# Kernel tuning notes

Measured on AMD Instinct MI355X. Metric: run time of the kernel, lower is better.

## Reference

```python
import jax, jax.numpy as jnp
import numpy as np

BATCH = 4096
DIM = 256
TEMP = 0.5
COS_EPS = 1e-8  # torch.nn.CosineSimilarity default eps


def setup_inputs() -> dict:
    key = jax.random.key(0)
    k1, k2 = jax.random.split(key)
    zis = jax.random.normal(k1, (BATCH, DIM), dtype=jnp.float32)
    zjs = jax.random.normal(k2, (BATCH, DIM), dtype=jnp.float32)
    return {"zis": zis, "zjs": zjs}


def reference(zis, zjs):
    n = zis.shape[0]  # batch_size
    # representations = cat([zjs, zis]) -> (2N, D)
    reps = jnp.concatenate([zjs, zis], axis=0)
    # cosine similarity matrix: dot / max(|x||y|, eps)  (matches torch CosineSimilarity)
    norms = jnp.linalg.norm(reps, axis=-1)  # (2N,)
    sim = (reps @ reps.T) / jnp.maximum(norms[:, None] * norms[None, :], COS_EPS)  # (2N, 2N)
    # positives: diag at offset +N (rows 0..N-1) then offset -N (rows N..2N-1)
    pos = jnp.concatenate([jnp.diagonal(sim, n), jnp.diagonal(sim, -n)])  # (2N,)
    # CE with label 0 over [pos, negatives]: negatives = row minus {diag, positive};
    # logsumexp([pos] + negatives) == logsumexp(row with only the self-diagonal masked),
    # since the positive appears exactly once in the row.
    two_n = 2 * n
    logits = sim / TEMP
    logits = jnp.where(jnp.eye(two_n, dtype=bool), -jnp.inf, logits)
    lse = jax.nn.logsumexp(logits, axis=-1)  # (2N,)
    loss = jnp.sum(lse - pos / TEMP)  # CrossEntropyLoss(reduction='sum')
    return loss / two_n
```

## Files before the change

kernel.cpp:

```cpp
#include <hip/hip_runtime.h>
#include <hip/hip_bf16.h>

#define TWO_N  8192
#define N_HALF 4096
#define DIMS   256

typedef __bf16 bf16x8 __attribute__((ext_vector_type(8)));
typedef float  f32x4  __attribute__((ext_vector_type(4)));
typedef unsigned short ushort8v __attribute__((ext_vector_type(8)));

__device__ __forceinline__ float fast_exp2(float x) {
#if __has_builtin(__builtin_amdgcn_exp2f)
    return __builtin_amdgcn_exp2f(x);
#else
    float r; asm("v_exp_f32 %0, %1" : "=v"(r) : "v"(x)); return r;
#endif
}

__global__ __launch_bounds__(256) void nrm_kernel(const float* __restrict__ zis,
                                                  const float* __restrict__ zjs,
                                                  unsigned short* __restrict__ swz)
{
    const int tid = threadIdx.x;
    const int l32 = tid & 31;
    const int row = blockIdx.x * 8 + (tid >> 5);
    const int k0  = l32 * 8;

    const float* src = (row < N_HALF) ? (zjs + (size_t)row * DIMS)
                                      : (zis + (size_t)(row - N_HALF) * DIMS);
    const float4 v0 = reinterpret_cast<const float4*>(src + k0)[0];
    const float4 v1 = reinterpret_cast<const float4*>(src + k0 + 4)[0];
    float ss = v0.x * v0.x + v0.y * v0.y + v0.z * v0.z + v0.w * v0.w
             + v1.x * v1.x + v1.y * v1.y + v1.z * v1.z + v1.w * v1.w;
#pragma unroll
    for (int m = 1; m < 32; m <<= 1) ss += __shfl_xor(ss, m, 64);
    const float inv = rsqrtf(ss) * 1.69864360045f;

    const float vals[8] = {v0.x, v0.y, v0.z, v0.w, v1.x, v1.y, v1.z, v1.w};
    ushort8v o;
#pragma unroll
    for (int j = 0; j < 8; ++j) {
        __hip_bfloat16 b = __float2bfloat16(vals[j] * inv);
        o[j] = *reinterpret_cast<unsigned short*>(&b);
    }
    const int chunk = ((row >> 4) * 8 + (l32 >> 2)) * 64 + (l32 & 3) * 16 + (row & 15);
    *reinterpret_cast<ushort8v*>(swz + (size_t)chunk * 8) = o;
}

__global__ __launch_bounds__(256, 2) void ntx_kernel(const __bf16* __restrict__ swz,
                                                     float* __restrict__ rowsum_part,
                                                     float* __restrict__ pos_part)
{
    const int lane = threadIdx.x & 63;
    const int wave = threadIdx.x >> 6;
    const int l15  = lane & 15;
    const int quad = lane >> 4;

    const int rg     = blockIdx.x & 31;
    const int cs     = blockIdx.x >> 5;
    const int wr0    = rg * 256 + wave * 64;
    const int c_base = cs * 256;
    const int p0     = wr0 ^ N_HALF;

    bf16x8 bfrag[4][8];
#pragma unroll
    for (int t = 0; t < 4; ++t) {
        const __bf16* bp = swz + (size_t)((wr0 >> 4) + t) * 4096 + lane * 8;
#pragma unroll
        for (int kk = 0; kk < 8; ++kk)
            bfrag[t][kk] = *reinterpret_cast<const bf16x8*>(bp + kk * 512);
    }

    const __bf16* abase = swz + (size_t)(cs * 16) * 4096 + lane * 8;

    float sum_exp[4] = {0.f, 0.f, 0.f, 0.f};
    float pos_acc = 0.f;

    bf16x8 a0[8], a1[8];
#pragma unroll
    for (int kk = 0; kk < 8; ++kk)
        a0[kk] = *reinterpret_cast<const bf16x8*>(abase + kk * 512);

    auto compute = [&](const bf16x8* af, int it) {
        const int c0 = c_base + it * 16;
        f32x4 acc[4] = {{0.f, 0.f, 0.f, 0.f}, {0.f, 0.f, 0.f, 0.f},
                        {0.f, 0.f, 0.f, 0.f}, {0.f, 0.f, 0.f, 0.f}};
#pragma unroll
        for (int kk = 0; kk < 8; ++kk) {
#pragma unroll
            for (int t = 0; t < 4; ++t)
                acc[t] = __builtin_amdgcn_mfma_f32_16x16x32_bf16(
                    af[kk], bfrag[t][kk], acc[t], 0, 0, 0);
        }
        const bool special = (c0 < wr0 + 64 && c0 + 16 > wr0) ||
                             (c0 < p0 + 64 && c0 + 16 > p0);
        if (!special) {
#pragma unroll
            for (int t = 0; t < 4; ++t)
#pragma unroll
                for (int j = 0; j < 4; ++j)
                    sum_exp[t] += fast_exp2(acc[t][j]);
        } else {
#pragma unroll
            for (int t = 0; t < 4; ++t) {
                const int r = wr0 + t * 16 + l15;
#pragma unroll
                for (int j = 0; j < 4; ++j) {
                    const int c = c0 + quad * 4 + j;
                    const float e = fast_exp2(acc[t][j]);
                    sum_exp[t] += (c == r) ? 0.f : e;
                    if (c == (r ^ N_HALF)) pos_acc += acc[t][j];
                }
            }
        }
    };

    for (int it = 0; it < 16; it += 2) {
#pragma unroll
        for (int kk = 0; kk < 8; ++kk)
            a1[kk] = *reinterpret_cast<const bf16x8*>(abase + (size_t)(it + 1) * 4096 + kk * 512);
        compute(a0, it);
        if (it + 2 < 16) {
#pragma unroll
            for (int kk = 0; kk < 8; ++kk)
                a0[kk] = *reinterpret_cast<const bf16x8*>(abase + (size_t)(it + 2) * 4096 + kk * 512);
        }
        compute(a1, it + 1);
    }

#pragma unroll
    for (int t = 0; t < 4; ++t) {
        float s = sum_exp[t];
        s += __shfl_xor(s, 16, 64);
        s += __shfl_xor(s, 32, 64);
        if (lane < 16)
            rowsum_part[(size_t)cs * TWO_N + wr0 + t * 16 + lane] = s;
    }

#pragma unroll
    for (int m = 1; m < 64; m <<= 1) pos_acc += __shfl_xor(pos_acc, m, 64);
    if (lane == 0) pos_part[blockIdx.x * 4 + wave] = pos_acc;
}

__global__ __launch_bounds__(1024) void fin1_kernel(const float* __restrict__ rowsum_part,
                                                    const float* __restrict__ pos_part,
                                                    float* __restrict__ block_part)
{
    __shared__ float red[16];
    const int t = threadIdx.x;
    const int r = blockIdx.x * 1024 + t;
    float acc = 0.f;
#pragma unroll
    for (int cs = 0; cs < 32; ++cs)
        acc += rowsum_part[(size_t)cs * TWO_N + r];
    float v = logf(acc);
    if (t < 512)
        v -= 0.69314718055994531f * pos_part[blockIdx.x * 512 + t];
#pragma unroll
    for (int m = 1; m < 64; m <<= 1) v += __shfl_xor(v, m, 64);
    if ((t & 63) == 0) red[t >> 6] = v;
    __syncthreads();
    if (t == 0) {
        float s = 0.f;
#pragma unroll
        for (int w = 0; w < 16; ++w) s += red[w];
        block_part[blockIdx.x] = s;
    }
}

__global__ void fin2_kernel(const float* __restrict__ block_part, float* __restrict__ out)
{
    if (threadIdx.x == 0) {
        float s = 0.f;
#pragma unroll
        for (int i = 0; i < 8; ++i) s += block_part[i];
        out[0] = s / (float)TWO_N;
    }
}

extern "C" void kernel_launch(void* const* d_in, const int* in_sizes, int n_in,
                              void* d_out, int out_size, void* d_ws, size_t ws_size,
                              hipStream_t stream)
{
    const float* zis = (const float*)d_in[0];
    const float* zjs = (const float*)d_in[1];

    unsigned short* swz = (unsigned short*)d_ws;
    float* rowsum_part  = (float*)((char*)d_ws + (size_t)TWO_N * DIMS * sizeof(unsigned short));
    float* pos_part     = rowsum_part + (size_t)32 * TWO_N;
    float* block_part   = pos_part + 4096;

    nrm_kernel<<<TWO_N / 8, 256, 0, stream>>>(zis, zjs, swz);
    ntx_kernel<<<1024, 256, 0, stream>>>((const __bf16*)swz, rowsum_part, pos_part);
    fin1_kernel<<<8, 1024, 0, stream>>>(rowsum_part, pos_part, block_part);
    fin2_kernel<<<1, 64, 0, stream>>>(block_part, (float*)d_out);
}
```

Measured before the change: 94.78 us.

## Exploit similarity-matrix symmetry by computing only upper-triangular block tiles

The grid is remapped from the full 32x32 set of row-group/column-group tiles to the 528 upper-triangular tiles. Each off-diagonal tile now also produces column-wise exp sums through lane shuffles and writes them to extra partial-sum slots, so the mirrored tile does not need its own MFMA and exp pass. The finish kernel gathers row partials and column partials per row group and doubles the weight on the positive term, since each positive pair is now seen once. The saving is roughly half the matmul and exp work, paid for with extra shuffles and global stores per 16-column step and a grid that no longer divides evenly across the CUs.

```diff
diff --git a/kernel.cpp b/kernel.cpp
--- a/kernel.cpp
+++ b/kernel.cpp
@@ -56,8 +56,11 @@
     const int l15  = lane & 15;
     const int quad = lane >> 4;
 
-    const int rg     = blockIdx.x & 31;
-    const int cs     = blockIdx.x >> 5;
+    int rg = 0, rem = blockIdx.x, width = 32;
+    while (rem >= width) { rem -= width; ++rg; --width; }
+    const int cs   = rg + rem;
+    const bool diag = (rg == cs);
+
     const int wr0    = rg * 256 + wave * 64;
     const int c_base = cs * 256;
     const int p0     = wr0 ^ N_HALF;
@@ -82,7 +85,7 @@
         a0[kk] = *reinterpret_cast<const bf16x8*>(abase + kk * 512);
 
     auto compute = [&](const bf16x8* af, int it) {
-        const int c0 = c_base + it * 16;
+        const int cc0 = c_base + it * 16;
         f32x4 acc[4] = {{0.f, 0.f, 0.f, 0.f}, {0.f, 0.f, 0.f, 0.f},
                         {0.f, 0.f, 0.f, 0.f}, {0.f, 0.f, 0.f, 0.f}};
 #pragma unroll
@@ -92,25 +95,49 @@
                 acc[t] = __builtin_amdgcn_mfma_f32_16x16x32_bf16(
                     af[kk], bfrag[t][kk], acc[t], 0, 0, 0);
         }
-        const bool special = (c0 < wr0 + 64 && c0 + 16 > wr0) ||
-                             (c0 < p0 + 64 && c0 + 16 > p0);
+        const bool special = (cc0 < wr0 + 64 && cc0 + 16 > wr0) ||
+                             (cc0 < p0 + 64 && cc0 + 16 > p0);
+        float pcol[4] = {0.f, 0.f, 0.f, 0.f};
         if (!special) {
 #pragma unroll
             for (int t = 0; t < 4; ++t)
 #pragma unroll
-                for (int j = 0; j < 4; ++j)
-                    sum_exp[t] += fast_exp2(acc[t][j]);
+                for (int j = 0; j < 4; ++j) {
+                    const float e = fast_exp2(acc[t][j]);
+                    sum_exp[t] += e;
+                    pcol[j] += e;
+                }
         } else {
 #pragma unroll
             for (int t = 0; t < 4; ++t) {
                 const int r = wr0 + t * 16 + l15;
 #pragma unroll
                 for (int j = 0; j < 4; ++j) {
-                    const int c = c0 + quad * 4 + j;
+                    const int c = cc0 + quad * 4 + j;
                     const float e = fast_exp2(acc[t][j]);
-                    sum_exp[t] += (c == r) ? 0.f : e;
+                    const bool self = (c == r);
+                    sum_exp[t] += self ? 0.f : e;
+                    pcol[j] += self ? 0.f : e;
                     if (c == (r ^ N_HALF)) pos_acc += acc[t][j];
                 }
+            }
+        }
+        if (!diag) {
+            const int b1 = lane & 1, b2 = lane & 2;
+            float a0v = b1 ? pcol[2] : pcol[0];
+            float g0v = b1 ? pcol[0] : pcol[2];
+            float a1v = b1 ? pcol[3] : pcol[1];
+            float g1v = b1 ? pcol[1] : pcol[3];
+            a0v += __shfl_xor(g0v, 1, 64);
+            a1v += __shfl_xor(g1v, 1, 64);
+            float k0v = b2 ? a1v : a0v;
+            float k1v = b2 ? a0v : a1v;
+            k0v += __shfl_xor(k1v, 2, 64);
+            k0v += __shfl_xor(k0v, 4, 64);
+            k0v += __shfl_xor(k0v, 8, 64);
+            if (l15 < 4) {
+                const int ccol = cc0 + quad * 4 + ((l15 & 1) * 2 + (l15 >> 1));
+                rowsum_part[(size_t)(32 + rg * 4 + wave) * TWO_N + ccol] = k0v;
             }
         }
     };
@@ -149,13 +176,16 @@
     __shared__ float red[16];
     const int t = threadIdx.x;
     const int r = blockIdx.x * 1024 + t;
+    const int g = r >> 8;
     float acc = 0.f;
-#pragma unroll
-    for (int cs = 0; cs < 32; ++cs)
-        acc += rowsum_part[(size_t)cs * TWO_N + r];
+    for (int s = g; s < 32; ++s)
+        acc += rowsum_part[(size_t)s * TWO_N + r];
+    const int ce = 32 + 4 * g;
+    for (int s = 32; s < ce; ++s)
+        acc += rowsum_part[(size_t)s * TWO_N + r];
     float v = logf(acc);
-    if (t < 512)
-        v -= 0.69314718055994531f * pos_part[blockIdx.x * 512 + t];
+    if (t < 264)
+        v -= 1.3862943611198906f * pos_part[blockIdx.x * 264 + t];
 #pragma unroll
     for (int m = 1; m < 64; m <<= 1) v += __shfl_xor(v, m, 64);
     if ((t & 63) == 0) red[t >> 6] = v;
@@ -187,11 +217,11 @@
 
     unsigned short* swz = (unsigned short*)d_ws;
     float* rowsum_part  = (float*)((char*)d_ws + (size_t)TWO_N * DIMS * sizeof(unsigned short));
-    float* pos_part     = rowsum_part + (size_t)32 * TWO_N;
-    float* block_part   = pos_part + 4096;
+    float* pos_part     = rowsum_part + (size_t)160 * TWO_N;
+    float* block_part   = pos_part + 2560;
 
     nrm_kernel<<<TWO_N / 8, 256, 0, stream>>>(zis, zjs, swz);
-    ntx_kernel<<<1024, 256, 0, stream>>>((const __bf16*)swz, rowsum_part, pos_part);
+    ntx_kernel<<<528, 256, 0, stream>>>((const __bf16*)swz, rowsum_part, pos_part);
     fin1_kernel<<<8, 1024, 0, stream>>>(rowsum_part, pos_part, block_part);
     fin2_kernel<<<1, 64, 0, stream>>>(block_part, (float*)d_out);
 }
```

Result: slower. 123.6 us (+30.4%).

## Exploit symmetry of similarity matrix to compute only upper-triangular tiles

Applied to the files above, without the earlier changes.

The GEMM now launches only the 496 strictly-upper block pairs (rg < cs) of the symmetric 2N×2N similarity matrix instead of all 1024 blocks. Each tile's exp values are reduced both by row and by column (the column sums go through a swizzled LDS buffer), so one tile feeds the row sums of both its row and column groups. Diagonal blocks are covered by an extra chunk MFMA path and a strip path with self-masking, and fin1 is changed to the new partial-sum layout and the doubled positive weight. This roughly halves the MFMA and exp work but adds a large LDS column buffer, extra syncs and irregular per-block work, which may reduce occupancy.

```diff
diff --git a/kernel.cpp b/kernel.cpp
--- a/kernel.cpp
+++ b/kernel.cpp
@@ -51,13 +51,29 @@
                                                      float* __restrict__ rowsum_part,
                                                      float* __restrict__ pos_part)
 {
-    const int lane = threadIdx.x & 63;
-    const int wave = threadIdx.x >> 6;
+    __shared__ float  colbuf[256 * 64];
+    __shared__ __bf16 chunkB[4096];
+    __shared__ float  cross[4][16];
+
+    const int tid  = threadIdx.x;
+    const int lane = tid & 63;
+    const int wave = tid >> 6;
     const int l15  = lane & 15;
     const int quad = lane >> 4;
 
-    const int rg     = blockIdx.x & 31;
-    const int cs     = blockIdx.x >> 5;
+    int rg = 0, rem = blockIdx.x, width = 31;
+    while (rem >= width) { rem -= width; ++rg; --width; }
+    const int cs = rg + 1 + rem;
+
+    const bool chunk_on = (rg < 16) && (cs >= 16);
+    const bool strip_on = (rg < 16) && (cs - rg <= 16);
+
+    if (chunk_on) {
+        const ushort8v* src = reinterpret_cast<const ushort8v*>(swz + (size_t)(cs * 16 + rg) * 4096);
+        reinterpret_cast<ushort8v*>(chunkB)[tid]       = src[tid];
+        reinterpret_cast<ushort8v*>(chunkB)[tid + 256] = src[tid + 256];
+    }
+
     const int wr0    = rg * 256 + wave * 64;
     const int c_base = cs * 256;
     const int p0     = wr0 ^ N_HALF;
@@ -74,7 +90,10 @@
     const __bf16* abase = swz + (size_t)(cs * 16) * 4096 + lane * 8;
 
     float sum_exp[4] = {0.f, 0.f, 0.f, 0.f};
-    float pos_acc = 0.f;
+    float pos_acc  = 0.f;
+    float chunkacc = 0.f;
+
+    __syncthreads();
 
     bf16x8 a0[8], a1[8];
 #pragma unroll
@@ -82,7 +101,7 @@
         a0[kk] = *reinterpret_cast<const bf16x8*>(abase + kk * 512);
 
     auto compute = [&](const bf16x8* af, int it) {
-        const int c0 = c_base + it * 16;
+        const int cc0 = c_base + it * 16;
         f32x4 acc[4] = {{0.f, 0.f, 0.f, 0.f}, {0.f, 0.f, 0.f, 0.f},
                         {0.f, 0.f, 0.f, 0.f}, {0.f, 0.f, 0.f, 0.f}};
 #pragma unroll
@@ -92,25 +111,54 @@
                 acc[t] = __builtin_amdgcn_mfma_f32_16x16x32_bf16(
                     af[kk], bfrag[t][kk], acc[t], 0, 0, 0);
         }
-        const bool special = (c0 < wr0 + 64 && c0 + 16 > wr0) ||
-                             (c0 < p0 + 64 && c0 + 16 > p0);
+        const bool special = (cc0 < p0 + 64 && cc0 + 16 > p0);
+        float pcol[4];
         if (!special) {
 #pragma unroll
-            for (int t = 0; t < 4; ++t)
-#pragma unroll
-                for (int j = 0; j < 4; ++j)
-                    sum_exp[t] += fast_exp2(acc[t][j]);
+            for (int j = 0; j < 4; ++j) {
+                float s = 0.f;
+#pragma unroll
+                for (int t = 0; t < 4; ++t) {
+                    const float e = fast_exp2(acc[t][j]);
+                    sum_exp[t] += e;
+                    s += e;
+                }
+                pcol[j] = s;
+            }
         } else {
+#pragma unroll
+            for (int j = 0; j < 4; ++j) pcol[j] = 0.f;
 #pragma unroll
             for (int t = 0; t < 4; ++t) {
                 const int r = wr0 + t * 16 + l15;
 #pragma unroll
                 for (int j = 0; j < 4; ++j) {
-                    const int c = c0 + quad * 4 + j;
+                    const int c = cc0 + quad * 4 + j;
                     const float e = fast_exp2(acc[t][j]);
-                    sum_exp[t] += (c == r) ? 0.f : e;
+                    sum_exp[t] += e;
+                    pcol[j] += e;
                     if (c == (r ^ N_HALF)) pos_acc += acc[t][j];
                 }
+            }
+        }
+#pragma unroll
+        for (int j = 0; j < 4; ++j) {
+            const int cl = it * 16 + quad * 4 + j;
+            colbuf[cl * 64 + ((wave * 16 + l15) ^ ((cl & 12) << 2))] = pcol[j];
+        }
+        if (chunk_on && (it >> 2) == wave) {
+            f32x4 accC = {0.f, 0.f, 0.f, 0.f};
+#pragma unroll
+            for (int kp = 0; kp < 4; ++kp) {
+                const bf16x8 b0 = *reinterpret_cast<const bf16x8*>(chunkB + (2 * kp)     * 512 + lane * 8);
+                const bf16x8 b1 = *reinterpret_cast<const bf16x8*>(chunkB + (2 * kp + 1) * 512 + lane * 8);
+                accC = __builtin_amdgcn_mfma_f32_16x16x32_bf16(af[2 * kp],     b0, accC, 0, 0, 0);
+                accC = __builtin_amdgcn_mfma_f32_16x16x32_bf16(af[2 * kp + 1], b1, accC, 0, 0, 0);
+            }
+#pragma unroll
+            for (int j = 0; j < 4; ++j) {
+                const bool self = (it == rg) && (quad * 4 + j == l15);
+                chunkacc += self ? 0.f : fast_exp2(accC[j]);
             }
         }
     };
@@ -140,6 +188,71 @@
 #pragma unroll
     for (int m = 1; m < 64; m <<= 1) pos_acc += __shfl_xor(pos_acc, m, 64);
     if (lane == 0) pos_part[blockIdx.x * 4 + wave] = pos_acc;
+
+    if (chunk_on) {
+        float s = chunkacc;
+        s += __shfl_xor(s, 16, 64);
+        s += __shfl_xor(s, 32, 64);
+        if (quad == 0) cross[wave][l15] = s;
+    }
+    __syncthreads();
+
+    {
+        const float4* cb = reinterpret_cast<const float4*>(colbuf + tid * 64);
+        float4 s4 = {0.f, 0.f, 0.f, 0.f};
+#pragma unroll
+        for (int i = 0; i < 16; ++i) {
+            const float4 v = cb[i ^ (tid & 12)];
+            s4.x += v.x; s4.y += v.y; s4.z += v.z; s4.w += v.w;
+        }
+        rowsum_part[(size_t)(32 + rg) * TWO_N + c_base + tid] =
+            (s4.x + s4.y) + (s4.z + s4.w);
+    }
+    if (chunk_on && tid < 16) {
+        const float s = cross[0][tid] + cross[1][tid] + cross[2][tid] + cross[3][tid];
+        rowsum_part[(size_t)cs * TWO_N + cs * 256 + rg * 16 + tid] = s;
+    }
+
+    if (strip_on) {
+        __syncthreads();
+        const int it0 = cs - rg - 1;
+        const __bf16* sb = swz + (size_t)(rg * 16 + it0) * 4096 + lane * 8;
+        bf16x8 as[8];
+#pragma unroll
+        for (int kk = 0; kk < 8; ++kk)
+            as[kk] = *reinterpret_cast<const bf16x8*>(sb + kk * 512);
+        f32x4 aS[4] = {{0.f, 0.f, 0.f, 0.f}, {0.f, 0.f, 0.f, 0.f},
+                       {0.f, 0.f, 0.f, 0.f}, {0.f, 0.f, 0.f, 0.f}};
+#pragma unroll
+        for (int kk = 0; kk < 8; ++kk) {
+#pragma unroll
+            for (int t = 0; t < 4; ++t)
+                aS[t] = __builtin_amdgcn_mfma_f32_16x16x32_bf16(
+                    as[kk], bfrag[t][kk], aS[t], 0, 0, 0);
+        }
+#pragma unroll
+        for (int j = 0; j < 4; ++j) {
+            float s = 0.f;
+#pragma unroll
+            for (int t = 0; t < 4; ++t) {
+                const bool self = ((wave * 4 + t) == it0) && (l15 == quad * 4 + j);
+                s += self ? 0.f : fast_exp2(aS[t][j]);
+            }
+            colbuf[(quad * 4 + j) * 64 + wave * 16 + l15] = s;
+        }
+        __syncthreads();
+        if (tid < 16) {
+            const float4* cb = reinterpret_cast<const float4*>(colbuf + tid * 64);
+            float4 s4 = {0.f, 0.f, 0.f, 0.f};
+#pragma unroll
+            for (int i = 0; i < 16; ++i) {
+                const float4 v = cb[i];
+                s4.x += v.x; s4.y += v.y; s4.z += v.z; s4.w += v.w;
+            }
+            rowsum_part[(size_t)rg * TWO_N + rg * 256 + it0 * 16 + tid] =
+                (s4.x + s4.y) + (s4.z + s4.w);
+        }
+    }
 }
 
 __global__ __launch_bounds__(1024) void fin1_kernel(const float* __restrict__ rowsum_part,
@@ -149,13 +262,16 @@
     __shared__ float red[16];
     const int t = threadIdx.x;
     const int r = blockIdx.x * 1024 + t;
+    const int g = r >> 8;
     float acc = 0.f;
-#pragma unroll
-    for (int cs = 0; cs < 32; ++cs)
-        acc += rowsum_part[(size_t)cs * TWO_N + r];
+    for (int s = g; s < 32; ++s)
+        acc += rowsum_part[(size_t)s * TWO_N + r];
+    const int ce = 32 + g;
+    for (int s = 32; s < ce; ++s)
+        acc += rowsum_part[(size_t)s * TWO_N + r];
     float v = logf(acc);
-    if (t < 512)
-        v -= 0.69314718055994531f * pos_part[blockIdx.x * 512 + t];
+    if (r < 1984)
+        v -= 1.3862943611198906f * pos_part[r];
 #pragma unroll
     for (int m = 1; m < 64; m <<= 1) v += __shfl_xor(v, m, 64);
     if ((t & 63) == 0) red[t >> 6] = v;
@@ -187,11 +303,11 @@
 
     unsigned short* swz = (unsigned short*)d_ws;
     float* rowsum_part  = (float*)((char*)d_ws + (size_t)TWO_N * DIMS * sizeof(unsigned short));
-    float* pos_part     = rowsum_part + (size_t)32 * TWO_N;
-    float* block_part   = pos_part + 4096;
+    float* pos_part     = rowsum_part + (size_t)64 * TWO_N;
+    float* block_part   = pos_part + 2048;
 
     nrm_kernel<<<TWO_N / 8, 256, 0, stream>>>(zis, zjs, swz);
-    ntx_kernel<<<1024, 256, 0, stream>>>((const __bf16*)swz, rowsum_part, pos_part);
+    ntx_kernel<<<496, 256, 0, stream>>>((const __bf16*)swz, rowsum_part, pos_part);
     fin1_kernel<<<8, 1024, 0, stream>>>(rowsum_part, pos_part, block_part);
     fin2_kernel<<<1, 64, 0, stream>>>(block_part, (float*)d_out);
 }
```

Result: slower. 98.83 us (+4.3%).

## Stage shared A tiles through LDS with async global-to-LDS loads

Applied to the files above, without the earlier changes.

Each wave previously loaded the full 16-column A tile from global memory into registers, so all four waves in a block fetched the same data. Now the four waves cooperatively load the tile into a double-buffered LDS array using global_load_lds, and each wave then reads its fragments from LDS. This cuts redundant global/L2 traffic and frees registers from the a0/a1 double buffer. In exchange it adds a block-wide barrier and a full vmcnt wait every iteration, which may serialize the load and compute stages.

```diff
diff --git a/kernel.cpp b/kernel.cpp
--- a/kernel.cpp
+++ b/kernel.cpp
@@ -17,6 +17,11 @@
 #endif
 }
 
+#define GLOAD_LDS16(g, l)                                                      \
+    __builtin_amdgcn_global_load_lds(                                          \
+        (const __attribute__((address_space(1))) unsigned int*)(g),            \
+        (__attribute__((address_space(3))) unsigned int*)(l), 16, 0, 0)
+
 __global__ __launch_bounds__(256) void nrm_kernel(const float* __restrict__ zis,
                                                   const float* __restrict__ zjs,
                                                   unsigned short* __restrict__ swz)
@@ -51,6 +56,8 @@
                                                      float* __restrict__ rowsum_part,
                                                      float* __restrict__ pos_part)
 {
+    __shared__ __bf16 abuf[2][4096];
+
     const int lane = threadIdx.x & 63;
     const int wave = threadIdx.x >> 6;
     const int l15  = lane & 15;
@@ -62,6 +69,16 @@
     const int c_base = cs * 256;
     const int p0     = wr0 ^ N_HALF;
 
+    auto stage = [&](int b, int it) {
+        const __bf16* gsrc = swz + (size_t)(cs * 16 + it) * 4096
+                           + (size_t)(wave * 2) * 512 + lane * 8;
+#pragma unroll
+        for (int h = 0; h < 2; ++h)
+            GLOAD_LDS16(gsrc + h * 512, &abuf[b][(wave * 2 + h) * 512]);
+    };
+
+    stage(0, 0);
+
     bf16x8 bfrag[4][8];
 #pragma unroll
     for (int t = 0; t < 4; ++t) {
@@ -71,17 +88,21 @@
             bfrag[t][kk] = *reinterpret_cast<const bf16x8*>(bp + kk * 512);
     }
 
-    const __bf16* abase = swz + (size_t)(cs * 16) * 4096 + lane * 8;
-
     float sum_exp[4] = {0.f, 0.f, 0.f, 0.f};
     float pos_acc = 0.f;
 
-    bf16x8 a0[8], a1[8];
-#pragma unroll
-    for (int kk = 0; kk < 8; ++kk)
-        a0[kk] = *reinterpret_cast<const bf16x8*>(abase + kk * 512);
-
-    auto compute = [&](const bf16x8* af, int it) {
+    asm volatile("s_waitcnt vmcnt(0)" ::: "memory");
+    __syncthreads();
+
+    int cur = 0;
+    for (int it = 0; it < 16; ++it) {
+        if (it + 1 < 16) stage(cur ^ 1, it + 1);
+
+        bf16x8 a[8];
+#pragma unroll
+        for (int kk = 0; kk < 8; ++kk)
+            a[kk] = *reinterpret_cast<const bf16x8*>(&abuf[cur][kk * 512 + lane * 8]);
+
         const int c0 = c_base + it * 16;
         f32x4 acc[4] = {{0.f, 0.f, 0.f, 0.f}, {0.f, 0.f, 0.f, 0.f},
                         {0.f, 0.f, 0.f, 0.f}, {0.f, 0.f, 0.f, 0.f}};
@@ -90,7 +111,7 @@
 #pragma unroll
             for (int t = 0; t < 4; ++t)
                 acc[t] = __builtin_amdgcn_mfma_f32_16x16x32_bf16(
-                    af[kk], bfrag[t][kk], acc[t], 0, 0, 0);
+                    a[kk], bfrag[t][kk], acc[t], 0, 0, 0);
         }
         const bool special = (c0 < wr0 + 64 && c0 + 16 > wr0) ||
                              (c0 < p0 + 64 && c0 + 16 > p0);
@@ -113,19 +134,10 @@
                 }
             }
         }
-    };
-
-    for (int it = 0; it < 16; it += 2) {
-#pragma unroll
-        for (int kk = 0; kk < 8; ++kk)
-            a1[kk] = *reinterpret_cast<const bf16x8*>(abase + (size_t)(it + 1) * 4096 + kk * 512);
-        compute(a0, it);
-        if (it + 2 < 16) {
-#pragma unroll
-            for (int kk = 0; kk < 8; ++kk)
-                a0[kk] = *reinterpret_cast<const bf16x8*>(abase + (size_t)(it + 2) * 4096 + kk * 512);
-        }
-        compute(a1, it + 1);
+
+        asm volatile("s_waitcnt vmcnt(0)" ::: "memory");
+        __syncthreads();
+        cur ^= 1;
     }
 
 #pragma unroll
```

Measured after the change: 100.4 us. 1.06x slower.
